# Kernel tuning notes

Measured on AMD Instinct MI355X. Metric: run time of the kernel, lower is better.

The kernel has to match this reference:

```python
import jax, jax.numpy as jnp
import numpy as np

SEQ, D, N = 8192, 1024, 4096

def setup_inputs() -> dict:
    key = jax.random.key(0)
    kx, kw, kb = jax.random.split(key, 3)
    x = jax.random.normal(kx, (SEQ, D), dtype=jnp.float32)
    W = jax.random.normal(kw, (N, D), dtype=jnp.float32) * (1.0 / np.sqrt(D))
    b = jax.random.normal(kb, (N,), dtype=jnp.float32) * 0.01
    return {"x": x, "W": W, "b": b}

def reference(x, W, b):
    # Each NEURON computes tanh(w . e + b_i); stacking over neurons and
    # over the embedding list is a single fused matmul + bias + activation.
    # out: [seq, numNeurons]
    return jnp.tanh(jnp.einsum('sd,nd->sn', x, W) + b)
```

## Files before the change

kernel.cpp:

```cpp
#include <hip/hip_runtime.h>
#include <hip/hip_fp16.h>

#define SEQ 8192
#define DIM 1024
#define NN  4096
#define KEFF 2048
#define NT   32
#define A_BYTES ((size_t)SEQ * KEFF * 2)
#define B_BYTES ((size_t)NN * DIM * 2)

using f16x8 = __attribute__((ext_vector_type(8))) _Float16;
using f16x4 = __attribute__((ext_vector_type(4))) _Float16;
using f32x4 = __attribute__((ext_vector_type(4))) float;

typedef __attribute__((address_space(1))) unsigned char as1_u8;
typedef __attribute__((address_space(3))) unsigned char as3_u8;

__device__ __forceinline__ float fast_tanh(float x) {
    float e = __expf(2.0f * x);
    return 1.0f - 2.0f / (e + 1.0f);
}

__global__ __launch_bounds__(256) void convert_kernel(
        const float* __restrict__ x, const float* __restrict__ w,
        f16x4* __restrict__ A, f16x4* __restrict__ B) {
    const int tid = threadIdx.x;
    const int b   = blockIdx.x;
    if (b < 8192) {
        const int gid = b * 256 + tid;
        const int s   = gid >> 8;
        const int c   = gid & 255;
        const float4 v = ((const float4*)x)[(size_t)s * 256 + c];
        const float f[4] = {v.x, v.y, v.z, v.w};
        f16x4 hv, lv;
#pragma unroll
        for (int e = 0; e < 4; e++) {
            const _Float16 h = (_Float16)f[e];
            hv[e] = h;
            lv[e] = (_Float16)(f[e] - (float)h);
        }
        f16x4* dst = A + (size_t)s * 512 + c;
        dst[0]   = hv;
        dst[256] = lv;
    } else {
        const int gid = (b - 8192) * 256 + tid;
        const int n   = gid >> 8;
        const int c   = gid & 255;
        const float4 v = ((const float4*)w)[(size_t)n * 256 + c];
        const float f[4] = {v.x, v.y, v.z, v.w};
        f16x4 hv;
#pragma unroll
        for (int e = 0; e < 4; e++) hv[e] = (_Float16)f[e];
        B[(size_t)n * 256 + c] = hv;
    }
}

__global__ __launch_bounds__(512, 1) void gemm_tanh_kernel(
        const _Float16* __restrict__ A,
        const _Float16* __restrict__ B,
        const float* __restrict__ bias,
        float* __restrict__ out) {
    __shared__ _Float16 lds[65536];

    const int tid  = threadIdx.x;
    const int lane = tid & 63;
    const int wave = tid >> 6;
    const int wm   = wave >> 2;
    const int wn   = wave & 3;
    const int l15  = lane & 15;
    const int lq   = lane >> 4;

    const int wgid = ((blockIdx.x & 7) << 6) | (blockIdx.x >> 3);
    const int qb = wgid >> 5;
    const int pb = wgid & 31;
    const int rowBase = pb << 8;
    const int colBase = qb << 8;

    const int sw  = l15 & 7;
    const int gk0 = ((lq)     ^ sw) << 4;
    const int gk1 = ((4 + lq) ^ sw) << 4;
    const int aOff = wm * 2048 + l15 * 128;
    const int bOff = 32768 + wn * 2048 + l15 * 128;

    const int srow = tid >> 3;
    const int sg   = (tid & 7) ^ (srow & 7);
    const unsigned ldsWave = (unsigned)wave << 10;

    const _Float16* Ag = A + (size_t)(rowBase + srow) * KEFF + sg * 8;
    const _Float16* Bg = B + (size_t)(colBase + srow) * DIM  + sg * 8;
    char* ldsc = (char*)lds;

    auto stageA = [&](int kt, int h, int d) {
        const _Float16* g = Ag + (size_t)h * 128 * KEFF + kt * 64;
        const unsigned lo = (unsigned)d * 65536u + (unsigned)h * 16384u + ldsWave;
        __builtin_amdgcn_global_load_lds((const as1_u8*)g,
                                         (as3_u8*)(ldsc + lo), 16, 0, 0);
        __builtin_amdgcn_global_load_lds((const as1_u8*)(g + (size_t)64 * KEFF),
                                         (as3_u8*)(ldsc + lo + 8192), 16, 0, 0);
    };
    auto stageB = [&](int kt, int h, int d) {
        const _Float16* g = Bg + (size_t)h * 128 * DIM + (kt & 15) * 64;
        const unsigned lo = (unsigned)d * 65536u + 32768u + (unsigned)h * 16384u + ldsWave;
        __builtin_amdgcn_global_load_lds((const as1_u8*)g,
                                         (as3_u8*)(ldsc + lo), 16, 0, 0);
        __builtin_amdgcn_global_load_lds((const as1_u8*)(g + (size_t)64 * DIM),
                                         (as3_u8*)(ldsc + lo + 8192), 16, 0, 0);
    };

    f32x4 acc[8][4] = {};
    f16x8 aH0[4][2], aH1[4][2], bN01[2][2], bN23[2][2];

    stageA(0, 0, 0); stageA(0, 1, 0); stageB(0, 0, 0); stageB(0, 1, 0);
    asm volatile("s_waitcnt vmcnt(0)" ::: "memory");
    __builtin_amdgcn_sched_barrier(0);
    __builtin_amdgcn_s_barrier();
    __builtin_amdgcn_sched_barrier(0);
#pragma unroll
    for (int i = 0; i < 4; ++i) {
        aH0[i][0] = *(const f16x8*)(ldsc + aOff + i * 4096 + gk0);
        aH0[i][1] = *(const f16x8*)(ldsc + aOff + i * 4096 + gk1);
    }
#pragma unroll
    for (int j = 0; j < 2; ++j) {
        bN01[j][0] = *(const f16x8*)(ldsc + bOff + j * 8192 + gk0);
        bN01[j][1] = *(const f16x8*)(ldsc + bOff + j * 8192 + gk1);
    }

    for (int t = 0; t < NT; ++t) {
        const int d  = t & 1;
        const int dn = d ^ 1;
        const char* lb  = ldsc + d * 65536;
        const char* lbn = ldsc + dn * 65536;

        if (t + 1 < NT) {
            stageA(t + 1, 0, dn); stageA(t + 1, 1, dn);
            stageB(t + 1, 0, dn); stageB(t + 1, 1, dn);
        }

#pragma unroll
        for (int j = 0; j < 2; ++j) {
            bN23[j][0] = *(const f16x8*)(lb + bOff + 16384 + j * 8192 + gk0);
            bN23[j][1] = *(const f16x8*)(lb + bOff + 16384 + j * 8192 + gk1);
        }
        __builtin_amdgcn_s_setprio(1);
#pragma unroll
        for (int k = 0; k < 2; ++k)
#pragma unroll
            for (int i = 0; i < 4; ++i)
#pragma unroll
                for (int j = 0; j < 2; ++j)
                    acc[i][j] = __builtin_amdgcn_mfma_f32_16x16x32_f16(
                        aH0[i][k], bN01[j][k], acc[i][j], 0, 0, 0);
        __builtin_amdgcn_s_setprio(0);

#pragma unroll
        for (int i = 0; i < 4; ++i) {
            aH1[i][0] = *(const f16x8*)(lb + aOff + 16384 + i * 4096 + gk0);
            aH1[i][1] = *(const f16x8*)(lb + aOff + 16384 + i * 4096 + gk1);
        }
        __builtin_amdgcn_s_setprio(1);
#pragma unroll
        for (int k = 0; k < 2; ++k)
#pragma unroll
            for (int i = 0; i < 4; ++i)
#pragma unroll
                for (int j = 0; j < 2; ++j)
                    acc[i][2 + j] = __builtin_amdgcn_mfma_f32_16x16x32_f16(
                        aH0[i][k], bN23[j][k], acc[i][2 + j], 0, 0, 0);
        __builtin_amdgcn_s_setprio(0);

        asm volatile("s_waitcnt lgkmcnt(0)" ::: "memory");
        __builtin_amdgcn_sched_barrier(0);
        asm volatile("s_waitcnt vmcnt(0)" ::: "memory");
        __builtin_amdgcn_sched_barrier(0);
        __builtin_amdgcn_s_barrier();
        __builtin_amdgcn_sched_barrier(0);

        if (t + 1 < NT) {
#pragma unroll
            for (int i = 0; i < 4; ++i) {
                aH0[i][0] = *(const f16x8*)(lbn + aOff + i * 4096 + gk0);
                aH0[i][1] = *(const f16x8*)(lbn + aOff + i * 4096 + gk1);
            }
        }
        __builtin_amdgcn_s_setprio(1);
#pragma unroll
        for (int k = 0; k < 2; ++k)
#pragma unroll
            for (int i = 0; i < 4; ++i)
#pragma unroll
                for (int j = 0; j < 2; ++j)
                    acc[4 + i][j] = __builtin_amdgcn_mfma_f32_16x16x32_f16(
                        aH1[i][k], bN01[j][k], acc[4 + i][j], 0, 0, 0);
        __builtin_amdgcn_s_setprio(0);

        if (t + 1 < NT) {
#pragma unroll
            for (int j = 0; j < 2; ++j) {
                bN01[j][0] = *(const f16x8*)(lbn + bOff + j * 8192 + gk0);
                bN01[j][1] = *(const f16x8*)(lbn + bOff + j * 8192 + gk1);
            }
        }
        __builtin_amdgcn_s_setprio(1);
#pragma unroll
        for (int k = 0; k < 2; ++k)
#pragma unroll
            for (int i = 0; i < 4; ++i)
#pragma unroll
                for (int j = 0; j < 2; ++j)
                    acc[4 + i][2 + j] = __builtin_amdgcn_mfma_f32_16x16x32_f16(
                        aH1[i][k], bN23[j][k], acc[4 + i][2 + j], 0, 0, 0);
        __builtin_amdgcn_s_setprio(0);
    }

#pragma unroll
    for (int j = 0; j < 4; ++j) {
        const int col = colBase + (j * 4 + wn) * 16 + l15;
        const float bj = bias[col];
#pragma unroll
        for (int r = 0; r < 8; ++r) {
            const size_t rb = (size_t)(rowBase + (r * 2 + wm) * 16 + lq * 4) * NN + col;
#pragma unroll
            for (int v = 0; v < 4; ++v)
                out[rb + (size_t)v * NN] = fast_tanh(acc[r][j][v] + bj);
        }
    }
}

__global__ void naive_gemm_kernel(const float* __restrict__ x,
                                  const float* __restrict__ W,
                                  const float* __restrict__ b,
                                  float* __restrict__ out) {
    __shared__ float xs[16][17], ws[16][17];
    int n = blockIdx.x * 16 + threadIdx.x;
    int m = blockIdx.y * 16 + threadIdx.y;
    float s = 0.f;
    for (int k0 = 0; k0 < DIM; k0 += 16) {
        xs[threadIdx.y][threadIdx.x] = x[(size_t)m * DIM + k0 + threadIdx.x];
        ws[threadIdx.y][threadIdx.x] =
            W[(size_t)(blockIdx.x * 16 + threadIdx.y) * DIM + k0 + threadIdx.x];
        __syncthreads();
#pragma unroll
        for (int kk = 0; kk < 16; kk++) s += xs[threadIdx.y][kk] * ws[threadIdx.x][kk];
        __syncthreads();
    }
    out[(size_t)m * NN + n] = tanhf(s + b[n]);
}

extern "C" void kernel_launch(void* const* d_in, const int* in_sizes, int n_in,
                              void* d_out, int out_size, void* d_ws, size_t ws_size,
                              hipStream_t stream) {
    const float* x = (const float*)d_in[0];
    const float* W = (const float*)d_in[1];
    const float* b = (const float*)d_in[2];
    float* out = (float*)d_out;

    const size_t need = A_BYTES + B_BYTES;
    if (ws_size < need) {
        dim3 grid(NN / 16, SEQ / 16), block(16, 16);
        naive_gemm_kernel<<<grid, block, 0, stream>>>(x, W, b, out);
        return;
    }

    _Float16* Abuf = (_Float16*)d_ws;
    _Float16* Bbuf = Abuf + (size_t)SEQ * KEFF;

    convert_kernel<<<12288, 256, 0, stream>>>(x, W, (f16x4*)Abuf, (f16x4*)Bbuf);

    gemm_tanh_kernel<<<512, 512, 0, stream>>>(Abuf, Bbuf, b, out);
}
```

Measured before the change: 280.2 us.

## Load B fragments directly from global into registers, halve LDS to allow two blocks

Drops the LDS staging of the B (weight) tile: each lane now reads its f16x8 B fragments straight from global memory into registers. A keeps its double-buffered LDS path. With only A in shared memory, the LDS footprint halves and launch bounds allow two blocks per CU, aiming for more occupancy and less LDS traffic. The trade-off is that B reads become per-lane 16-byte global loads that are not shared across waves and sit on the critical path with no async prefetch, so they may expose memory latency.

```diff
diff --git a/kernel.cpp b/kernel.cpp
--- a/kernel.cpp
+++ b/kernel.cpp
@@ -55,12 +55,12 @@
     }
 }
 
-__global__ __launch_bounds__(512, 1) void gemm_tanh_kernel(
+__global__ __launch_bounds__(512, 2) void gemm_tanh_kernel(
         const _Float16* __restrict__ A,
         const _Float16* __restrict__ B,
         const float* __restrict__ bias,
         float* __restrict__ out) {
-    __shared__ _Float16 lds[65536];
+    __shared__ _Float16 lds[32768];
 
     const int tid  = threadIdx.x;
     const int lane = tid & 63;
@@ -80,37 +80,29 @@
     const int gk0 = ((lq)     ^ sw) << 4;
     const int gk1 = ((4 + lq) ^ sw) << 4;
     const int aOff = wm * 2048 + l15 * 128;
-    const int bOff = 32768 + wn * 2048 + l15 * 128;
 
     const int srow = tid >> 3;
     const int sg   = (tid & 7) ^ (srow & 7);
     const unsigned ldsWave = (unsigned)wave << 10;
 
     const _Float16* Ag = A + (size_t)(rowBase + srow) * KEFF + sg * 8;
-    const _Float16* Bg = B + (size_t)(colBase + srow) * DIM  + sg * 8;
     char* ldsc = (char*)lds;
+
+    const _Float16* Bf = B + (size_t)(colBase + wn * 16 + l15) * DIM + lq * 8;
 
     auto stageA = [&](int kt, int h, int d) {
         const _Float16* g = Ag + (size_t)h * 128 * KEFF + kt * 64;
-        const unsigned lo = (unsigned)d * 65536u + (unsigned)h * 16384u + ldsWave;
+        const unsigned lo = (unsigned)d * 32768u + (unsigned)h * 16384u + ldsWave;
         __builtin_amdgcn_global_load_lds((const as1_u8*)g,
                                          (as3_u8*)(ldsc + lo), 16, 0, 0);
         __builtin_amdgcn_global_load_lds((const as1_u8*)(g + (size_t)64 * KEFF),
                                          (as3_u8*)(ldsc + lo + 8192), 16, 0, 0);
     };
-    auto stageB = [&](int kt, int h, int d) {
-        const _Float16* g = Bg + (size_t)h * 128 * DIM + (kt & 15) * 64;
-        const unsigned lo = (unsigned)d * 65536u + 32768u + (unsigned)h * 16384u + ldsWave;
-        __builtin_amdgcn_global_load_lds((const as1_u8*)g,
-                                         (as3_u8*)(ldsc + lo), 16, 0, 0);
-        __builtin_amdgcn_global_load_lds((const as1_u8*)(g + (size_t)64 * DIM),
-                                         (as3_u8*)(ldsc + lo + 8192), 16, 0, 0);
-    };
 
     f32x4 acc[8][4] = {};
     f16x8 aH0[4][2], aH1[4][2], bN01[2][2], bN23[2][2];
 
-    stageA(0, 0, 0); stageA(0, 1, 0); stageB(0, 0, 0); stageB(0, 1, 0);
+    stageA(0, 0, 0); stageA(0, 1, 0);
     asm volatile("s_waitcnt vmcnt(0)" ::: "memory");
     __builtin_amdgcn_sched_barrier(0);
     __builtin_amdgcn_s_barrier();
@@ -121,27 +113,26 @@
         aH0[i][1] = *(const f16x8*)(ldsc + aOff + i * 4096 + gk1);
     }
 #pragma unroll
-    for (int j = 0; j < 2; ++j) {
-        bN01[j][0] = *(const f16x8*)(ldsc + bOff + j * 8192 + gk0);
-        bN01[j][1] = *(const f16x8*)(ldsc + bOff + j * 8192 + gk1);
-    }
+    for (int j = 0; j < 2; ++j)
+#pragma unroll
+        for (int kk = 0; kk < 2; ++kk)
+            bN01[j][kk] = *(const f16x8*)(Bf + (size_t)j * 64 * DIM + kk * 32);
 
     for (int t = 0; t < NT; ++t) {
         const int d  = t & 1;
         const int dn = d ^ 1;
-        const char* lb  = ldsc + d * 65536;
-        const char* lbn = ldsc + dn * 65536;
-
-        if (t + 1 < NT) {
-            stageA(t + 1, 0, dn); stageA(t + 1, 1, dn);
-            stageB(t + 1, 0, dn); stageB(t + 1, 1, dn);
-        }
-
-#pragma unroll
-        for (int j = 0; j < 2; ++j) {
-            bN23[j][0] = *(const f16x8*)(lb + bOff + 16384 + j * 8192 + gk0);
-            bN23[j][1] = *(const f16x8*)(lb + bOff + 16384 + j * 8192 + gk1);
-        }
+        const char* lb  = ldsc + d * 32768;
+        const char* lbn = ldsc + dn * 32768;
+        const int toff  = (t & 15) * 64;
+
+        if (t + 1 < NT) { stageA(t + 1, 0, dn); stageA(t + 1, 1, dn); }
+
+#pragma unroll
+        for (int j = 0; j < 2; ++j)
+#pragma unroll
+            for (int kk = 0; kk < 2; ++kk)
+                bN23[j][kk] = *(const f16x8*)(Bf + (size_t)(2 + j) * 64 * DIM
+                                              + toff + kk * 32);
         __builtin_amdgcn_s_setprio(1);
 #pragma unroll
         for (int k = 0; k < 2; ++k)
@@ -195,11 +186,13 @@
         __builtin_amdgcn_s_setprio(0);
 
         if (t + 1 < NT) {
-#pragma unroll
-            for (int j = 0; j < 2; ++j) {
-                bN01[j][0] = *(const f16x8*)(lbn + bOff + j * 8192 + gk0);
-                bN01[j][1] = *(const f16x8*)(lbn + bOff + j * 8192 + gk1);
-            }
+            const int toffn = ((t + 1) & 15) * 64;
+#pragma unroll
+            for (int j = 0; j < 2; ++j)
+#pragma unroll
+                for (int kk = 0; kk < 2; ++kk)
+                    bN01[j][kk] = *(const f16x8*)(Bf + (size_t)j * 64 * DIM
+                                                  + toffn + kk * 32);
         }
         __builtin_amdgcn_s_setprio(1);
 #pragma unroll
```

Result: slower. 349.6 us (+24.8%).
